# Optimization experiments

Hardware: AMD Instinct MI355X
Metric: run time of the kernel (lower is better)

Reference implementation:

```python
import jax, jax.numpy as jnp
import numpy as np

B, N, F_IN, F_OUT, H = 4, 2048, 128, 256, 4
HD = F_OUT // H


def setup_inputs() -> dict:
    key = jax.random.key(0)
    k1, k2, k3, k4, k5 = jax.random.split(key, 5)
    x = jax.random.normal(k1, (B, N, F_IN), dtype=jnp.float32)
    adj = jax.random.randint(k2, (B, N, N), 0, 2, dtype=jnp.int32)
    # xavier-ish scaled params
    W = jax.random.normal(k3, (F_OUT, F_IN), dtype=jnp.float32) * float(np.sqrt(2.0 / (F_IN + F_OUT)))
    a_l = jax.random.normal(k4, (H, HD), dtype=jnp.float32) * float(np.sqrt(2.0 / (H * HD + 1)))
    a_r = jax.random.normal(k5, (H, HD), dtype=jnp.float32) * float(np.sqrt(2.0 / (H * HD + 1)))
    return {"x": x, "adj": adj, "W": W, "a_l": a_l, "a_r": a_r}


def reference(x, adj, W, a_l, a_r):
    Bb, Nn, _ = x.shape
    h = jnp.einsum('bnf,of->bno', x, W).reshape(Bb, Nn, H, HD)   # [B,N,H,HD]
    e_l = jnp.einsum('bnhd,hd->bnh', h, a_l)                      # [B,N,H]
    e_r = jnp.einsum('bnhd,hd->bnh', h, a_r)                      # [B,N,H]
    e = e_l[:, :, None, :] + e_r[:, None, :, :]                   # [B,N(i),N(j),H]
    e = jax.nn.leaky_relu(e, negative_slope=0.2)
    e = jnp.where(adj[..., None] == 0, -jnp.inf, e)
    alpha = jax.nn.softmax(e, axis=2)                             # softmax over neighbors j
    out = jnp.einsum('bijh,bjhd->bihd', alpha, h)                 # [B,N,H,HD]
    return out.reshape(Bb, Nn, F_OUT)
```

## Files before the change

### kernel.cpp

```cpp
#include <hip/hip_runtime.h>
#include <stdint.h>

#define BB 4
#define NN 2048
#define F_IN 128
#define F_OUT 256
#define NH 4
#define HD 64

typedef float f32x4 __attribute__((ext_vector_type(4)));
typedef float f32x2 __attribute__((ext_vector_type(2)));
typedef short s16x8 __attribute__((ext_vector_type(8)));
typedef int i32x4 __attribute__((ext_vector_type(4)));
typedef unsigned long long u64;
typedef unsigned short u16;

#define LOG2E 1.4426950408889634f

__device__ __forceinline__ u16 f32_to_bf16_rtn(float f) {
    union { float f; uint32_t u; } v; v.f = f;
    uint32_t u = v.u;
    u += 0x7fffu + ((u >> 16) & 1u);
    return (u16)(u >> 16);
}

__device__ __forceinline__ float exp2_fast(float x) {
#if __has_builtin(__builtin_amdgcn_exp2f)
    return __builtin_amdgcn_exp2f(x);
#else
    return exp2f(x);
#endif
}

__device__ __forceinline__ int sbfe1(uint32_t v, int k) {
#if __has_builtin(__builtin_amdgcn_sbfe)
    return __builtin_amdgcn_sbfe((int)v, k, 1);
#else
    return ((int32_t)(v << (31 - k))) >> 31;
#endif
}

__global__ __launch_bounds__(256) void k0_pack(
    const int* __restrict__ adj, u64* __restrict__ abits)
{
    const int t = threadIdx.x;
    const int row = (blockIdx.x << 2) | (t >> 6);
    const int lane = t & 63;
    const int* rowp = adj + (size_t)row * NN;
    u64 mym = 0;
    for (int g = 0; g < 4; ++g) {
        int v[8];
#pragma unroll
        for (int u = 0; u < 8; ++u) v[u] = rowp[(g * 8 + u) * 64 + lane];
#pragma unroll
        for (int u = 0; u < 8; ++u) {
            u64 m = __ballot(v[u] != 0);
            if (lane == g * 8 + u) mym = m;
        }
    }
    if (lane < 32) abits[(size_t)row * 32 + lane] = mym;
}

__global__ __launch_bounds__(256) void k1_proj(
    const float* __restrict__ x, const float* __restrict__ W,
    const float* __restrict__ a_l, const float* __restrict__ a_r,
    u16* __restrict__ hB, float* __restrict__ el, f32x2* __restrict__ er12)
{
    const int t = threadIdx.x;

    __shared__ __align__(16) float red[4 * 64 * 20];
    float (*xs)[F_IN] = (float(*)[F_IN])red;

    const int b = blockIdx.x >> 7;
    const int n0 = (blockIdx.x & 127) * 16;

    {
        const f32x4* src = (const f32x4*)(x + ((size_t)b * NN + n0) * F_IN);
        f32x4* dst = (f32x4*)&xs[0][0];
        dst[t] = src[t];
        dst[t + 256] = src[t + 256];
    }
    __syncthreads();

    float acc[16];
#pragma unroll
    for (int n = 0; n < 16; ++n) acc[n] = 0.f;

    const float* wrow = W + (size_t)t * F_IN;
#pragma unroll 2
    for (int k0 = 0; k0 < F_IN; k0 += 8) {
        f32x4 w0 = *(const f32x4*)(wrow + k0);
        f32x4 w1 = *(const f32x4*)(wrow + k0 + 4);
#pragma unroll
        for (int n = 0; n < 16; ++n) {
            f32x4 xa = *(const f32x4*)&xs[n][k0];
            f32x4 xb = *(const f32x4*)&xs[n][k0 + 4];
            float s = acc[n];
            s = fmaf(xa[0], w0[0], s); s = fmaf(xa[1], w0[1], s);
            s = fmaf(xa[2], w0[2], s); s = fmaf(xa[3], w0[3], s);
            s = fmaf(xb[0], w1[0], s); s = fmaf(xb[1], w1[1], s);
            s = fmaf(xb[2], w1[2], s); s = fmaf(xb[3], w1[3], s);
            acc[n] = s;
        }
    }
    __syncthreads();

    const int w = t >> 6, lane = t & 63;
    const float al = a_l[t];
    const float ar = a_r[t];
    const int n_ = lane & 15, og = lane >> 4;
    float sl, sr;
    {
        float* rp = &red[((size_t)w * 64 + lane) * 20];
#pragma unroll
        for (int q = 0; q < 4; ++q) {
            f32x4 v;
#pragma unroll
            for (int e = 0; e < 4; ++e) v[e] = acc[q * 4 + e] * al;
            *(f32x4*)(rp + q * 4) = v;
        }
    }
    __syncthreads();
    {
        float s = 0.f;
#pragma unroll
        for (int oo = 0; oo < 16; ++oo)
            s += red[((size_t)w * 64 + og + 4 * oo) * 20 + n_];
        s += __shfl_xor(s, 16, 64); s += __shfl_xor(s, 32, 64);
        sl = s;
    }
    __syncthreads();
    {
        float* rp = &red[((size_t)w * 64 + lane) * 20];
#pragma unroll
        for (int q = 0; q < 4; ++q) {
            f32x4 v;
#pragma unroll
            for (int e = 0; e < 4; ++e) v[e] = acc[q * 4 + e] * ar;
            *(f32x4*)(rp + q * 4) = v;
        }
    }
    __syncthreads();
    {
        float s = 0.f;
#pragma unroll
        for (int oo = 0; oo < 16; ++oo)
            s += red[((size_t)w * 64 + og + 4 * oo) * 20 + n_];
        s += __shfl_xor(s, 16, 64); s += __shfl_xor(s, 32, 64);
        sr = s;
    }
    if (lane < 16) {
        el[((size_t)b * NH + w) * NN + n0 + lane] = sl * LOG2E;
        float sre = sr * LOG2E;
        f32x2 v2; v2[0] = exp2_fast(sre); v2[1] = exp2_fast(0.2f * sre);
        er12[((size_t)b * NH + w) * NN + n0 + lane] = v2;
    }

    const int dcol = t & 15, cb = (t >> 4) & 3;
    const int jt32 = n0 >> 5;
    const int lb = dcol + ((n0 >> 3) & 2) * 16;
    u16* hb = hB + ((((size_t)b * 64 + jt32) * 4 + w) * 4 + cb) * 512 + (size_t)lb * 8;
    s16x8 pk0, pk1;
#pragma unroll
    for (int n = 0; n < 8; ++n) pk0[n] = (short)f32_to_bf16_rtn(acc[n]);
#pragma unroll
    for (int n = 0; n < 8; ++n) pk1[n] = (short)f32_to_bf16_rtn(acc[n + 8]);
    *(s16x8*)hb         = pk0;
    *(s16x8*)(hb + 128) = pk1;
}

#define MSTRIDE 68

__global__ __launch_bounds__(256, 3) void k2_attn(
    const uint32_t* __restrict__ abits32, const u16* __restrict__ hB,
    const float* __restrict__ el, const f32x2* __restrict__ er12,
    float* __restrict__ out)
{
    __shared__ __align__(16) char smem[33792];
    float*    er_lds   = (float*)smem;
    uint32_t* mask_lds = (uint32_t*)(smem + 16384);
    float*    racc     = (float*)smem;

    const int t = threadIdx.x;
    const int jq = t >> 6, l = t & 63;
    const int o = blockIdx.x;
    const int kblk = o >> 3;
    const int bw = (o & 7) + 8 * (kblk & 1);
    const int b = bw >> 2;
    const int w = bw & 3;
    const int i0 = (kblk >> 1) * 32;
    const int r = l & 15;
    const int kb = l >> 4;
    const int ks = kb * 8;
    const int irow0 = i0 + r, irow1 = irow0 + 16;

    {
        const f32x4* gsrc = (const f32x4*)(er12 + (size_t)(b * NH + w) * NN);
        f32x4* edst = (f32x4*)er_lds;
#pragma unroll
        for (int p = 0; p < 4; ++p) edst[t + p * 256] = gsrc[t + p * 256];
        const i32x4* msrc = (const i32x4*)(abits32 + ((size_t)b * NN + i0) * 64);
        i32x4 mv0 = msrc[t * 2];
        i32x4 mv1 = msrc[t * 2 + 1];
        const int mrow = t >> 3, mc = (t & 7) * 8;
        *(i32x4*)&mask_lds[mrow * MSTRIDE + mc]     = mv0;
        *(i32x4*)&mask_lds[mrow * MSTRIDE + mc + 4] = mv1;
    }

    const u16* hbp = hB + ((((size_t)b * 64 + jq * 16) * 4 + w) * 4) * 512 + (size_t)l * 8;
    const float eli0 = el[((size_t)b * NH + w) * NN + irow0];
    const float eli1 = el[((size_t)b * NH + w) * NN + irow1];
    const float E1i0 = exp2_fast(eli0), E2i0 = exp2_fast(0.2f * eli0);
    const float E1i1 = exp2_fast(eli1), E2i1 = exp2_fast(0.2f * eli1);

    f32x4 a00 = {0.f,0.f,0.f,0.f}, a01 = a00, a02 = a00, a03 = a00, as0 = a00;
    f32x4 a10 = a00, a11 = a00, a12 = a00, a13 = a00, as1 = a00;
    s16x8 ones;
#pragma unroll
    for (int k = 0; k < 8; ++k) ones[k] = (short)0x3F80;

    s16x8 b0c = *(const s16x8*)(hbp + 0 * 512);
    s16x8 b1c = *(const s16x8*)(hbp + 1 * 512);
    s16x8 b2c = *(const s16x8*)(hbp + 2 * 512);
    s16x8 b3c = *(const s16x8*)(hbp + 3 * 512);
    __syncthreads();

#define MFMA_BF16 __builtin_amdgcn_mfma_f32_16x16x32_bf16
#define BODY(IT, PF)                                                          \
    {                                                                         \
        const int itv = (IT);                                                 \
        const int jb2 = (jq * 512 + itv * 32 + ks) * 2;                       \
        f32x4 e0 = *(const f32x4*)(er_lds + jb2);                             \
        f32x4 e1 = *(const f32x4*)(er_lds + jb2 + 4);                         \
        f32x4 e2 = *(const f32x4*)(er_lds + jb2 + 8);                         \
        f32x4 e3 = *(const f32x4*)(er_lds + jb2 + 12);                        \
        uint32_t w2a = mask_lds[r * MSTRIDE + jq * 16 + itv] >> ks;           \
        uint32_t w2b = mask_lds[(16 + r) * MSTRIDE + jq * 16 + itv] >> ks;    \
        s16x8 b0n, b1n, b2n, b3n;                                             \
        if (PF) {                                                             \
            const u16* hp_ = hbp + (size_t)(itv + 1) * 8192;                  \
            b0n = *(const s16x8*)(hp_ + 0 * 512);                             \
            b1n = *(const s16x8*)(hp_ + 1 * 512);                             \
            b2n = *(const s16x8*)(hp_ + 2 * 512);                             \
            b3n = *(const s16x8*)(hp_ + 3 * 512);                             \
        }                                                                     \
        __builtin_amdgcn_sched_barrier(0);                                    \
        union { s16x8 v; uint32_t u[4]; } afa, afb;                           \
        _Pragma("unroll")                                                     \
        for (int kk = 0; kk < 4; ++kk) {                                      \
            f32x4 ev = (kk == 0) ? e0 : ((kk == 1) ? e1 : ((kk == 2) ? e2 : e3)); \
            float t00 = E1i0 * ev[0], m00 = E2i0 * ev[1];                     \
            float t01 = E1i0 * ev[2], m01 = E2i0 * ev[3];                     \
            float t10 = E1i1 * ev[0], m10 = E2i1 * ev[1];                     \
            float t11 = E1i1 * ev[2], m11 = E2i1 * ev[3];                     \
            float p00 = fmaxf(t00, m00);           \
            float p01 = fmaxf(t01, m01);                                      \
            float p10 = fmaxf(t10, m10);                                      \
            float p11 = fmaxf(t11, m11);                                      \
            union { float f; uint32_t u; } c00, c01, c10, c11;                \
            c00.f = p00; c01.f = p01; c10.f = p10; c11.f = p11;               \
            uint32_t q00 = c00.u & (uint32_t)sbfe1(w2a, 2 * kk);              \
            uint32_t q01 = c01.u & (uint32_t)sbfe1(w2a, 2 * kk + 1);          \
            uint32_t q10 = c10.u & (uint32_t)sbfe1(w2b, 2 * kk);              \
            uint32_t q11 = c11.u & (uint32_t)sbfe1(w2b, 2 * kk + 1);          \
            afa.u[kk] = __builtin_amdgcn_perm(q01, q00, 0x07060302);          \
            afb.u[kk] = __builtin_amdgcn_perm(q11, q10, 0x07060302);          \
        }                                                                     \
        a00 = MFMA_BF16(afa.v, b0c, a00, 0, 0, 0);                            \
        a01 = MFMA_BF16(afa.v, b1c, a01, 0, 0, 0);                            \
        a02 = MFMA_BF16(afa.v, b2c, a02, 0, 0, 0);                            \
        a03 = MFMA_BF16(afa.v, b3c, a03, 0, 0, 0);                            \
        as0 = MFMA_BF16(afa.v, ones, as0, 0, 0, 0);                           \
        a10 = MFMA_BF16(afb.v, b0c, a10, 0, 0, 0);                            \
        a11 = MFMA_BF16(afb.v, b1c, a11, 0, 0, 0);                            \
        a12 = MFMA_BF16(afb.v, b2c, a12, 0, 0, 0);                            \
        a13 = MFMA_BF16(afb.v, b3c, a13, 0, 0, 0);                            \
        as1 = MFMA_BF16(afb.v, ones, as1, 0, 0, 0);                           \
        if (PF) { b0c = b0n; b1c = b1n; b2c = b2n; b3c = b3n; }               \
    }

    for (int g = 0; g < 3; ++g) {
#pragma unroll
        for (int s = 0; s < 4; ++s) BODY(g * 4 + s, 1);
    }
    BODY(12, 1); BODY(13, 1); BODY(14, 1); BODY(15, 0);

    __syncthreads();
    if (jq > 0) {
        float* p = &racc[((jq - 1) * 64 + l) * 44];
        *(f32x4*)(p +  0) = a00; *(f32x4*)(p +  4) = a01;
        *(f32x4*)(p +  8) = a02; *(f32x4*)(p + 12) = a03;
        *(f32x4*)(p + 16) = as0;
        *(f32x4*)(p + 20) = a10; *(f32x4*)(p + 24) = a11;
        *(f32x4*)(p + 28) = a12; *(f32x4*)(p + 32) = a13;
        *(f32x4*)(p + 36) = as1;
    }
    __syncthreads();
    if (jq == 0) {
#pragma unroll
        for (int s = 0; s < 3; ++s) {
            const float* p = &racc[(s * 64 + l) * 44];
            a00 += *(const f32x4*)(p +  0); a01 += *(const f32x4*)(p +  4);
            a02 += *(const f32x4*)(p +  8); a03 += *(const f32x4*)(p + 12);
            as0 += *(const f32x4*)(p + 16);
            a10 += *(const f32x4*)(p + 20); a11 += *(const f32x4*)(p + 24);
            a12 += *(const f32x4*)(p + 28); a13 += *(const f32x4*)(p + 32);
            as1 += *(const f32x4*)(p + 36);
        }

        float* op = out + ((size_t)b * NN + i0) * F_OUT + w * HD;
#pragma unroll
        for (int q = 0; q < 4; ++q) {
            const int row0 = kb * 4 + q;
            float inv0 = 1.0f / as0[q];
            __builtin_nontemporal_store(a00[q] * inv0, &op[(size_t)row0 * F_OUT +  0 + r]);
            __builtin_nontemporal_store(a01[q] * inv0, &op[(size_t)row0 * F_OUT + 16 + r]);
            __builtin_nontemporal_store(a02[q] * inv0, &op[(size_t)row0 * F_OUT + 32 + r]);
            __builtin_nontemporal_store(a03[q] * inv0, &op[(size_t)row0 * F_OUT + 48 + r]);
            const int row1 = 16 + kb * 4 + q;
            float inv1 = 1.0f / as1[q];
            __builtin_nontemporal_store(a10[q] * inv1, &op[(size_t)row1 * F_OUT +  0 + r]);
            __builtin_nontemporal_store(a11[q] * inv1, &op[(size_t)row1 * F_OUT + 16 + r]);
            __builtin_nontemporal_store(a12[q] * inv1, &op[(size_t)row1 * F_OUT + 32 + r]);
            __builtin_nontemporal_store(a13[q] * inv1, &op[(size_t)row1 * F_OUT + 48 + r]);
        }
    }
}

extern "C" void kernel_launch(void* const* d_in, const int* in_sizes, int n_in,
                              void* d_out, int out_size, void* d_ws, size_t ws_size,
                              hipStream_t stream) {
    const float* x   = (const float*)d_in[0];
    const int*   adj = (const int*)d_in[1];
    const float* W   = (const float*)d_in[2];
    const float* a_l = (const float*)d_in[3];
    const float* a_r = (const float*)d_in[4];
    float* out = (float*)d_out;

    char* ws = (char*)d_ws;
    u16*      hB      = (u16*)ws;
    u64*      abits   = (u64*)(ws + (size_t)BB * F_OUT * NN * 2);
    float*    el      = (float*)(ws + (size_t)BB * F_OUT * NN * 2 + (size_t)BB * NN * 256);
    f32x2*    er12    = (f32x2*)(el + (size_t)BB * NH * NN);

    k0_pack<<<BB * NN / 4, 256, 0, stream>>>(adj, abits);
    k1_proj<<<BB * (NN / 16), 256, 0, stream>>>(x, W, a_l, a_r, hB, el, er12);
    k2_attn<<<BB * NH * (NN / 32), 256, 0, stream>>>((const uint32_t*)abits, hB, el, er12, out);
}
```

Before: 50.89 us.

## Fuse adjacency bit-packing into attention kernel with two heads per block

Removes the separate pack kernel and has the attention kernel read the int32 adjacency tile directly and build the bitmask in shared memory. Each block now covers two heads, with waves split into head and neighbor halves, so every packed mask tile serves two heads and the grid is halved. The intent is to drop one launch and the round trip of the packed mask through global memory. The cost is that the adjacency matrix is now read twice overall (once per head pair), shared memory grows, and each wave runs a longer j loop.

```diff
diff --git a/kernel.cpp b/kernel.cpp
--- a/kernel.cpp
+++ b/kernel.cpp
@@ -38,27 +38,6 @@
 #else
     return ((int32_t)(v << (31 - k))) >> 31;
 #endif
-}
-
-__global__ __launch_bounds__(256) void k0_pack(
-    const int* __restrict__ adj, u64* __restrict__ abits)
-{
-    const int t = threadIdx.x;
-    const int row = (blockIdx.x << 2) | (t >> 6);
-    const int lane = t & 63;
-    const int* rowp = adj + (size_t)row * NN;
-    u64 mym = 0;
-    for (int g = 0; g < 4; ++g) {
-        int v[8];
-#pragma unroll
-        for (int u = 0; u < 8; ++u) v[u] = rowp[(g * 8 + u) * 64 + lane];
-#pragma unroll
-        for (int u = 0; u < 8; ++u) {
-            u64 m = __ballot(v[u] != 0);
-            if (lane == g * 8 + u) mym = m;
-        }
-    }
-    if (lane < 32) abits[(size_t)row * 32 + lane] = mym;
 }
 
 __global__ __launch_bounds__(256) void k1_proj(
@@ -170,44 +149,61 @@
 }
 
 #define MSTRIDE 68
-
-__global__ __launch_bounds__(256, 3) void k2_attn(
-    const uint32_t* __restrict__ abits32, const u16* __restrict__ hB,
+#define ER_F32  8192
+#define SMEM_B  (ER_F32 * 4 + 32 * MSTRIDE * 4)
+
+__global__ __launch_bounds__(256, 3) void k2_fused(
+    const int* __restrict__ adj, const u16* __restrict__ hB,
     const float* __restrict__ el, const f32x2* __restrict__ er12,
     float* __restrict__ out)
 {
-    __shared__ __align__(16) char smem[33792];
+    __shared__ __align__(16) char smem[SMEM_B];
     float*    er_lds   = (float*)smem;
-    uint32_t* mask_lds = (uint32_t*)(smem + 16384);
+    uint32_t* mask_lds = (uint32_t*)(smem + ER_F32 * 4);
     float*    racc     = (float*)smem;
 
     const int t = threadIdx.x;
-    const int jq = t >> 6, l = t & 63;
+    const int wave = t >> 6, l = t & 63;
+    const int wsub = wave & 1;
+    const int jh = wave >> 1;
     const int o = blockIdx.x;
-    const int kblk = o >> 3;
-    const int bw = (o & 7) + 8 * (kblk & 1);
-    const int b = bw >> 2;
-    const int w = bw & 3;
-    const int i0 = (kblk >> 1) * 32;
+    const int xcd = o & 7;
+    const int b = xcd >> 1;
+    const int hp = xcd & 1;
+    const int i0 = (o >> 3) * 32;
+    const int w = hp * 2 + wsub;
     const int r = l & 15;
     const int kb = l >> 4;
     const int ks = kb * 8;
     const int irow0 = i0 + r, irow1 = irow0 + 16;
 
     {
-        const f32x4* gsrc = (const f32x4*)(er12 + (size_t)(b * NH + w) * NN);
+        const int* adjb = adj + ((size_t)b * NN + i0) * NN;
+#pragma unroll
+        for (int p = 0; p < 8; ++p) {
+            const int m = t + p * 256;
+            const int row = m >> 6, wd = m & 63;
+            const i32x4* wp = (const i32x4*)(adjb + (size_t)row * NN + wd * 32);
+            i32x4 v[8];
+#pragma unroll
+            for (int u = 0; u < 8; ++u) v[u] = wp[u];
+            uint32_t word = 0;
+#pragma unroll
+            for (int u = 0; u < 8; ++u) {
+#pragma unroll
+                for (int e = 0; e < 4; ++e)
+                    word |= (uint32_t)(v[u][e] != 0) << (4 * u + e);
+            }
+            mask_lds[row * MSTRIDE + wd] = word;
+        }
+        const f32x4* gsrc = (const f32x4*)(er12 + ((size_t)b * NH + hp * 2) * NN);
         f32x4* edst = (f32x4*)er_lds;
 #pragma unroll
-        for (int p = 0; p < 4; ++p) edst[t + p * 256] = gsrc[t + p * 256];
-        const i32x4* msrc = (const i32x4*)(abits32 + ((size_t)b * NN + i0) * 64);
-        i32x4 mv0 = msrc[t * 2];
-        i32x4 mv1 = msrc[t * 2 + 1];
-        const int mrow = t >> 3, mc = (t & 7) * 8;
-        *(i32x4*)&mask_lds[mrow * MSTRIDE + mc]     = mv0;
-        *(i32x4*)&mask_lds[mrow * MSTRIDE + mc + 4] = mv1;
-    }
-
-    const u16* hbp = hB + ((((size_t)b * 64 + jq * 16) * 4 + w) * 4) * 512 + (size_t)l * 8;
+        for (int p = 0; p < 8; ++p) edst[t + p * 256] = gsrc[t + p * 256];
+    }
+
+    const u16* hbp = hB + ((((size_t)b * 64 + jh * 32) * 4 + w) * 4) * 512 + (size_t)l * 8;
+    const float* erw = er_lds + wsub * (2 * NN);
     const float eli0 = el[((size_t)b * NH + w) * NN + irow0];
     const float eli1 = el[((size_t)b * NH + w) * NN + irow1];
     const float E1i0 = exp2_fast(eli0), E2i0 = exp2_fast(0.2f * eli0);
@@ -229,13 +225,13 @@
 #define BODY(IT, PF)                                                          \
     {                                                                         \
         const int itv = (IT);                                                 \
-        const int jb2 = (jq * 512 + itv * 32 + ks) * 2;                       \
-        f32x4 e0 = *(const f32x4*)(er_lds + jb2);                             \
-        f32x4 e1 = *(const f32x4*)(er_lds + jb2 + 4);                         \
-        f32x4 e2 = *(const f32x4*)(er_lds + jb2 + 8);                         \
-        f32x4 e3 = *(const f32x4*)(er_lds + jb2 + 12);                        \
-        uint32_t w2a = mask_lds[r * MSTRIDE + jq * 16 + itv] >> ks;           \
-        uint32_t w2b = mask_lds[(16 + r) * MSTRIDE + jq * 16 + itv] >> ks;    \
+        const int jb2 = (itv * 32 + ks) * 2;                                  \
+        f32x4 e0 = *(const f32x4*)(erw + jh * 2048 + jb2);                    \
+        f32x4 e1 = *(const f32x4*)(erw + jh * 2048 + jb2 + 4);                \
+        f32x4 e2 = *(const f32x4*)(erw + jh * 2048 + jb2 + 8);                \
+        f32x4 e3 = *(const f32x4*)(erw + jh * 2048 + jb2 + 12);               \
+        uint32_t w2a = mask_lds[r * MSTRIDE + jh * 32 + itv] >> ks;           \
+        uint32_t w2b = mask_lds[(16 + r) * MSTRIDE + jh * 32 + itv] >> ks;    \
         s16x8 b0n, b1n, b2n, b3n;                                             \
         if (PF) {                                                             \
             const u16* hp_ = hbp + (size_t)(itv + 1) * 8192;                  \
@@ -279,15 +275,15 @@
         if (PF) { b0c = b0n; b1c = b1n; b2c = b2n; b3c = b3n; }               \
     }
 
-    for (int g = 0; g < 3; ++g) {
+    for (int g = 0; g < 7; ++g) {
 #pragma unroll
         for (int s = 0; s < 4; ++s) BODY(g * 4 + s, 1);
     }
-    BODY(12, 1); BODY(13, 1); BODY(14, 1); BODY(15, 0);
-
-    __syncthreads();
-    if (jq > 0) {
-        float* p = &racc[((jq - 1) * 64 + l) * 44];
+    BODY(28, 1); BODY(29, 1); BODY(30, 1); BODY(31, 0);
+
+    __syncthreads();
+    if (jh == 1) {
+        float* p = &racc[((size_t)(wsub * 64 + l)) * 44];
         *(f32x4*)(p +  0) = a00; *(f32x4*)(p +  4) = a01;
         *(f32x4*)(p +  8) = a02; *(f32x4*)(p + 12) = a03;
         *(f32x4*)(p + 16) = as0;
@@ -296,17 +292,14 @@
         *(f32x4*)(p + 36) = as1;
     }
     __syncthreads();
-    if (jq == 0) {
-#pragma unroll
-        for (int s = 0; s < 3; ++s) {
-            const float* p = &racc[(s * 64 + l) * 44];
-            a00 += *(const f32x4*)(p +  0); a01 += *(const f32x4*)(p +  4);
-            a02 += *(const f32x4*)(p +  8); a03 += *(const f32x4*)(p + 12);
-            as0 += *(const f32x4*)(p + 16);
-            a10 += *(const f32x4*)(p + 20); a11 += *(const f32x4*)(p + 24);
-            a12 += *(const f32x4*)(p + 28); a13 += *(const f32x4*)(p + 32);
-            as1 += *(const f32x4*)(p + 36);
-        }
+    if (jh == 0) {
+        const float* p = &racc[((size_t)(wsub * 64 + l)) * 44];
+        a00 += *(const f32x4*)(p +  0); a01 += *(const f32x4*)(p +  4);
+        a02 += *(const f32x4*)(p +  8); a03 += *(const f32x4*)(p + 12);
+        as0 += *(const f32x4*)(p + 16);
+        a10 += *(const f32x4*)(p + 20); a11 += *(const f32x4*)(p + 24);
+        a12 += *(const f32x4*)(p + 28); a13 += *(const f32x4*)(p + 32);
+        as1 += *(const f32x4*)(p + 36);
 
         float* op = out + ((size_t)b * NN + i0) * F_OUT + w * HD;
 #pragma unroll
@@ -338,12 +331,10 @@
     float* out = (float*)d_out;
 
     char* ws = (char*)d_ws;
-    u16*      hB      = (u16*)ws;
-    u64*      abits   = (u64*)(ws + (size_t)BB * F_OUT * NN * 2);
-    float*    el      = (float*)(ws + (size_t)BB * F_OUT * NN * 2 + (size_t)BB * NN * 256);
-    f32x2*    er12    = (f32x2*)(el + (size_t)BB * NH * NN);
-
-    k0_pack<<<BB * NN / 4, 256, 0, stream>>>(adj, abits);
+    u16*   hB   = (u16*)ws;
+    float* el   = (float*)(ws + (size_t)BB * F_OUT * NN * 2);
+    f32x2* er12 = (f32x2*)(el + (size_t)BB * NH * NN);
+
     k1_proj<<<BB * (NN / 16), 256, 0, stream>>>(x, W, a_l, a_r, hB, el, er12);
-    k2_attn<<<BB * NH * (NN / 32), 256, 0, stream>>>((const uint32_t*)abits, hB, el, er12, out);
-}
+    k2_fused<<<BB * 2 * (NN / 32), 256, 0, stream>>>(adj, hB, el, er12, out);
+}
```

Result: slower. 59.66 us (+17.2%).
